# Optimization experiments

Hardware: AMD Instinct MI355X
Metric: run time of the kernel (lower is better)

## Reference

```python
import jax, jax.numpy as jnp
import numpy as np

C = 1024
H = 16
EPS = 1e-5

def layernorm(x, g, b):
    mu = jnp.mean(x, axis=-1, keepdims=True)
    var = jnp.var(x, axis=-1, keepdims=True)
    return (x - mu) * jax.lax.rsqrt(var + EPS) * g + b

def setup_inputs() -> dict:
    key = jax.random.key(0)
    ks = jax.random.split(key, 12)
    s = lambda fan: 1.0 / np.sqrt(fan)
    return {
        "x": jax.random.normal(ks[0], (2, 2048, C), jnp.float32),
        "W_qkv": jax.random.uniform(ks[1], (C, 3 * C), jnp.float32, -s(C), s(C)),
        "W_o": jax.random.uniform(ks[2], (C, C), jnp.float32, -s(C), s(C)),
        "b_o": jnp.zeros((C,), jnp.float32),
        "g1": jnp.ones((C,), jnp.float32),
        "beta1": jnp.zeros((C,), jnp.float32),
        "g2": jnp.ones((C,), jnp.float32),
        "beta2": jnp.zeros((C,), jnp.float32),
        "W_ff1": jax.random.uniform(ks[3], (C, 4 * C), jnp.float32, -s(C), s(C)),
        "b_ff1": jnp.zeros((4 * C,), jnp.float32),
        "W_ff2": jax.random.uniform(ks[4], (4 * C, C), jnp.float32, -s(4 * C), s(4 * C)),
        "b_ff2": jnp.zeros((C,), jnp.float32),
    }

def reference(x, W_qkv, W_o, b_o, g1, beta1, g2, beta2, W_ff1, b_ff1, W_ff2, b_ff2):
    B, T, _ = x.shape
    hd = C // H  # head dim
    # --- self-attention on norm1(x) ---
    h = layernorm(x, g1, beta1)
    qkv = h @ W_qkv                      # [B,T,3C]
    q, k, v = jnp.split(qkv, 3, axis=-1)
    reshp = lambda t: t.reshape(B, T, H, hd).transpose(0, 2, 1, 3)  # [B,H,T,hd]
    q, k, v = reshp(q), reshp(k), reshp(v)
    att = jnp.einsum("bhqd,bhkd->bhqk", q, k) * (hd ** -0.5)
    causal = jnp.tril(jnp.ones((T, T), bool))
    att = jnp.where(causal, att, -jnp.inf)
    att = jax.nn.softmax(att, axis=-1)
    out = jnp.einsum("bhqk,bhkd->bhqd", att, v)
    out = out.transpose(0, 2, 1, 3).reshape(B, T, C)
    x = x + out @ W_o + b_o
    # --- feed-forward on norm2(x) ---
    h = layernorm(x, g2, beta2)
    h = jax.nn.relu(h @ W_ff1 + b_ff1) @ W_ff2 + b_ff2
    return x + h
```

## Files before the change

### kernel.cpp

```cpp
#include <hip/hip_runtime.h>
#include <hip/hip_bf16.h>
#include <stdint.h>


typedef __attribute__((ext_vector_type(8))) short bf16x8;
typedef __attribute__((ext_vector_type(4))) float f32x4;

#define MFMA16(a, b, c) __builtin_amdgcn_mfma_f32_16x16x32_bf16((a), (b), (c), 0, 0, 0)

__device__ __forceinline__ void gload16(const void* g, void* l) {
    __builtin_amdgcn_global_load_lds(
        (const __attribute__((address_space(1))) char*)g,
        (__attribute__((address_space(3))) char*)l, 16, 0, 0);
}

__global__ __launch_bounds__(256) void tconv_k(const float* __restrict__ in,
                                               __hip_bfloat16* __restrict__ out,
                                               int K, int N) {
    __shared__ float tile[32][33];
    const int n0 = blockIdx.x * 32, k0 = blockIdx.y * 32;
    const int tx = threadIdx.x, ty = threadIdx.y;
    for (int i = ty; i < 32; i += 8)
        tile[i][tx] = in[(size_t)(k0 + i) * N + n0 + tx];
    __syncthreads();
    for (int i = ty; i < 32; i += 8)
        out[(size_t)(n0 + i) * K + k0 + tx] = __float2bfloat16(tile[tx][i]);
}

__global__ __launch_bounds__(256) void ln_k(const float* __restrict__ x,
                                            const float* __restrict__ g,
                                            const float* __restrict__ beta,
                                            __hip_bfloat16* __restrict__ out) {
    const int row = blockIdx.x;
    const int tid = threadIdx.x;
    float4 v = ((const float4*)(x + (size_t)row * 1024))[tid];
    float s  = v.x + v.y + v.z + v.w;
    float s2 = v.x * v.x + v.y * v.y + v.z * v.z + v.w * v.w;
    for (int off = 1; off < 64; off <<= 1) {
        s  += __shfl_xor(s,  off, 64);
        s2 += __shfl_xor(s2, off, 64);
    }
    __shared__ float ss[4], ss2[4];
    const int w = tid >> 6, lane = tid & 63;
    if (lane == 0) { ss[w] = s; ss2[w] = s2; }
    __syncthreads();
    s  = ss[0] + ss[1] + ss[2] + ss[3];
    s2 = ss2[0] + ss2[1] + ss2[2] + ss2[3];
    const float mu  = s * (1.0f / 1024.0f);
    const float var = s2 * (1.0f / 1024.0f) - mu * mu;
    const float rs  = rsqrtf(var + 1e-5f);
    float4 gv = ((const float4*)g)[tid];
    float4 bv = ((const float4*)beta)[tid];
    __hip_bfloat16* o = out + (size_t)row * 1024 + tid * 4;
    o[0] = __float2bfloat16((v.x - mu) * rs * gv.x + bv.x);
    o[1] = __float2bfloat16((v.y - mu) * rs * gv.y + bv.y);
    o[2] = __float2bfloat16((v.z - mu) * rs * gv.z + bv.z);
    o[3] = __float2bfloat16((v.w - mu) * rs * gv.w + bv.w);
}

template <int BIAS, int RELU, int RESID, int OUTBF>
__global__ __launch_bounds__(256, 3) void gemm_k(const __hip_bfloat16* __restrict__ A,
                                                 const __hip_bfloat16* __restrict__ Bt,
                                                 const float* __restrict__ bias,
                                                 const float* __restrict__ resid,
                                                 void* __restrict__ out,
                                                 int M, int N, int K) {
    __align__(16) __shared__ __hip_bfloat16 As[128 * 64];
    __align__(16) __shared__ __hip_bfloat16 Bs[128 * 64];

    const int tid  = threadIdx.x;
    const int lane = tid & 63, w = tid >> 6;
    const int wm = w >> 1, wn = w & 1;
    const int m0 = blockIdx.y * 128, n0 = blockIdx.x * 128;
    const int l16 = lane & 15, quad = lane >> 4;

    const int srw = lane >> 3;
    const int scn = ((lane & 7) - srw) & 7;

    const __hip_bfloat16* ga[4];
    const __hip_bfloat16* gb[4];
#pragma unroll
    for (int i = 0; i < 4; i++) {
        const int row = i * 32 + w * 8 + srw;
        ga[i] = A  + (size_t)(m0 + row) * K + scn * 8;
        gb[i] = Bt + (size_t)(n0 + row) * K + scn * 8;
    }

    int offA[2][4], offB[2][4];
#pragma unroll
    for (int s = 0; s < 2; s++)
#pragma unroll
        for (int t = 0; t < 4; t++) {
            const int rA = wm * 64 + t * 16 + l16;
            offA[s][t] = (rA * 8 + ((s * 4 + quad + (rA & 7)) & 7)) * 16;
            const int rB = wn * 64 + t * 16 + l16;
            offB[s][t] = (rB * 8 + ((s * 4 + quad + (rB & 7)) & 7)) * 16;
        }

    f32x4 acc[4][4] = {};

    for (int k0 = 0; k0 < K; k0 += 64) {
        __syncthreads();
#pragma unroll
        for (int i = 0; i < 4; i++) {
            gload16(ga[i], As + (i * 256 + w * 64) * 8);
            gload16(gb[i], Bs + (i * 256 + w * 64) * 8);
            ga[i] += 64; gb[i] += 64;
        }
        __syncthreads();

#pragma unroll
        for (int s = 0; s < 2; s++) {
            bf16x8 af[4], bfr[4];
#pragma unroll
            for (int t = 0; t < 4; t++) {
                af[t]  = *(const bf16x8*)((const char*)As + offA[s][t]);
                bfr[t] = *(const bf16x8*)((const char*)Bs + offB[s][t]);
            }
#pragma unroll
            for (int mt = 0; mt < 4; mt++)
#pragma unroll
                for (int nt = 0; nt < 4; nt++)
                    acc[mt][nt] = MFMA16(af[mt], bfr[nt], acc[mt][nt]);
        }
    }

#pragma unroll
    for (int mt = 0; mt < 4; mt++)
#pragma unroll
        for (int nt = 0; nt < 4; nt++) {
            const int row = m0 + wm * 64 + mt * 16 + quad * 4;
            const int col = n0 + wn * 64 + nt * 16 + l16;
            const float bv = BIAS ? bias[col] : 0.0f;
#pragma unroll
            for (int r = 0; r < 4; r++) {
                float v = acc[mt][nt][r] + bv;
                if (RELU) v = v > 0.0f ? v : 0.0f;
                const size_t idx = (size_t)(row + r) * N + col;
                if (RESID) v += resid[idx];
                if (OUTBF) ((__hip_bfloat16*)out)[idx] = __float2bfloat16(v);
                else       ((float*)out)[idx] = v;
            }
        }
}

template <int BIAS, int RELU, int RESID, int OUTBF>
__global__ __launch_bounds__(256, 3) void gemm64_k(const __hip_bfloat16* __restrict__ A,
                                                   const __hip_bfloat16* __restrict__ Bt,
                                                   const float* __restrict__ bias,
                                                   const float* __restrict__ resid,
                                                   void* __restrict__ out,
                                                   int M, int N, int K) {
    __align__(16) __shared__ __hip_bfloat16 As[128 * 64];
    __align__(16) __shared__ __hip_bfloat16 Bs[64 * 64];

    const int tid  = threadIdx.x;
    const int lane = tid & 63, w = tid >> 6;
    const int wm = w >> 1, wn = w & 1;
    const int m0 = blockIdx.y * 128, n0 = blockIdx.x * 64;
    const int l16 = lane & 15, quad = lane >> 4;

    const int srw = lane >> 3;
    const int scn = ((lane & 7) - srw) & 7;

    const __hip_bfloat16* ga[4];
    const __hip_bfloat16* gb[2];
#pragma unroll
    for (int i = 0; i < 4; i++)
        ga[i] = A + (size_t)(m0 + i * 32 + w * 8 + srw) * K + scn * 8;
#pragma unroll
    for (int i = 0; i < 2; i++)
        gb[i] = Bt + (size_t)(n0 + i * 32 + w * 8 + srw) * K + scn * 8;

    int offA[2][4], offB[2][2];
#pragma unroll
    for (int s = 0; s < 2; s++) {
#pragma unroll
        for (int t = 0; t < 4; t++) {
            const int rA = wm * 64 + t * 16 + l16;
            offA[s][t] = (rA * 8 + ((s * 4 + quad + (rA & 7)) & 7)) * 16;
        }
#pragma unroll
        for (int t = 0; t < 2; t++) {
            const int rB = wn * 32 + t * 16 + l16;
            offB[s][t] = (rB * 8 + ((s * 4 + quad + (rB & 7)) & 7)) * 16;
        }
    }

    f32x4 acc[4][2] = {};

    for (int k0 = 0; k0 < K; k0 += 64) {
        __syncthreads();
#pragma unroll
        for (int i = 0; i < 4; i++) {
            gload16(ga[i], As + (i * 256 + w * 64) * 8);
            ga[i] += 64;
        }
#pragma unroll
        for (int i = 0; i < 2; i++) {
            gload16(gb[i], Bs + (i * 256 + w * 64) * 8);
            gb[i] += 64;
        }
        __syncthreads();

#pragma unroll
        for (int s = 0; s < 2; s++) {
            bf16x8 af[4], bfr[2];
#pragma unroll
            for (int t = 0; t < 4; t++)
                af[t] = *(const bf16x8*)((const char*)As + offA[s][t]);
#pragma unroll
            for (int t = 0; t < 2; t++)
                bfr[t] = *(const bf16x8*)((const char*)Bs + offB[s][t]);
#pragma unroll
            for (int mt = 0; mt < 4; mt++)
#pragma unroll
                for (int nt = 0; nt < 2; nt++)
                    acc[mt][nt] = MFMA16(af[mt], bfr[nt], acc[mt][nt]);
        }
    }

#pragma unroll
    for (int mt = 0; mt < 4; mt++)
#pragma unroll
        for (int nt = 0; nt < 2; nt++) {
            const int row = m0 + wm * 64 + mt * 16 + quad * 4;
            const int col = n0 + wn * 32 + nt * 16 + l16;
            const float bv = BIAS ? bias[col] : 0.0f;
#pragma unroll
            for (int r = 0; r < 4; r++) {
                float v = acc[mt][nt][r] + bv;
                if (RELU) v = v > 0.0f ? v : 0.0f;
                const size_t idx = (size_t)(row + r) * N + col;
                if (RESID) v += resid[idx];
                if (OUTBF) ((__hip_bfloat16*)out)[idx] = __float2bfloat16(v);
                else       ((float*)out)[idx] = v;
            }
        }
}

__global__ __launch_bounds__(256) void vtrans_k(const __hip_bfloat16* __restrict__ qkv,
                                                __hip_bfloat16* __restrict__ vt) {
    const int T = 2048, C3 = 3072;
    const int bh = blockIdx.y, b = bh >> 4, h = bh & 15;
    const int t0 = blockIdx.x * 64;
    const int tx = threadIdx.x, ty = threadIdx.y;
    __shared__ __hip_bfloat16 tile[64][65];
#pragma unroll
    for (int j = 0; j < 16; j++) {
        const int tl = ty * 16 + j;
        tile[tl][tx] = qkv[(size_t)(b * T + t0 + tl) * C3 + 2048 + h * 64 + tx];
    }
    __syncthreads();
#pragma unroll
    for (int j = 0; j < 16; j++) {
        const int d = ty * 16 + j;
        vt[((size_t)bh * 64 + d) * 2048 + t0 + tx] = tile[tx][d];
    }
}

__global__ __launch_bounds__(256, 3) void attn_k(const __hip_bfloat16* __restrict__ qkv,
                                                 const __hip_bfloat16* __restrict__ vt,
                                                 __hip_bfloat16* __restrict__ outp) {
    const int T = 2048, C3 = 3072;
    const int bh = blockIdx.x, b = bh >> 4, h = bh & 15;
    const int qt = 31 - blockIdx.y;
    const int q0 = qt * 64;
    const int tid = threadIdx.x, lane = tid & 63, w = tid >> 6;
    const int l16 = lane & 15, quad = lane >> 4;

    __align__(16) __shared__ __hip_bfloat16 Ks[2][64 * 64];
    __align__(16) __shared__ __hip_bfloat16 Vs[2][64 * 64];
    __align__(16) __shared__ __hip_bfloat16 Pw[4][16 * 72];

    const float sc = 0.125f * 1.44269504f;
    bf16x8 qf0, qf1;
    {
        const __hip_bfloat16* qp =
            qkv + (size_t)(b * T + q0 + w * 16 + l16) * C3 + h * 64;
        bf16x8 a = *(const bf16x8*)(qp + quad * 8);
        bf16x8 c = *(const bf16x8*)(qp + 32 + quad * 8);
#pragma unroll
        for (int i = 0; i < 8; i++) {
            union { unsigned int u; float f; } ua, uc;
            ua.u = ((unsigned int)(unsigned short)a[i]) << 16;
            uc.u = ((unsigned int)(unsigned short)c[i]) << 16;
            qf0[i] = (short)(__bfloat16_as_ushort(__float2bfloat16(ua.f * sc)));
            qf1[i] = (short)(__bfloat16_as_ushort(__float2bfloat16(uc.f * sc)));
        }
    }

    const int srw = lane >> 3;
    const int scn = ((lane & 7) - srw) & 7;
    const __hip_bfloat16* kp[2];
    const __hip_bfloat16* vp[2];
#pragma unroll
    for (int i = 0; i < 2; i++) {
        const int row = i * 32 + w * 8 + srw;
        kp[i] = qkv + (size_t)(b * T + row) * C3 + 1024 + h * 64 + scn * 8;
        vp[i] = vt + ((size_t)bh * 64 + row) * 2048 + scn * 8;
    }

    int offK[2][4], offV[2][4];
#pragma unroll
    for (int s = 0; s < 2; s++)
#pragma unroll
        for (int t = 0; t < 4; t++) {
            const int rr = t * 16 + l16;
            const int o = (rr * 8 + ((s * 4 + quad + (rr & 7)) & 7)) * 16;
            offK[s][t] = o;
            offV[s][t] = o;
        }

    f32x4 oacc[4] = {};
    float lpart[4] = {0.0f, 0.0f, 0.0f, 0.0f};

#pragma unroll
    for (int i = 0; i < 2; i++) {
        gload16(kp[i], Ks[0] + (i * 256 + w * 64) * 8);
        gload16(vp[i], Vs[0] + (i * 256 + w * 64) * 8);
    }

    for (int kt = 0; kt <= qt; kt++) {
        const int buf = kt & 1;
        __syncthreads();
        if (kt < qt) {
#pragma unroll
            for (int i = 0; i < 2; i++) {
                gload16(kp[i] + (size_t)(kt + 1) * 64 * C3,
                        Ks[buf ^ 1] + (i * 256 + w * 64) * 8);
                gload16(vp[i] + (kt + 1) * 64,
                        Vs[buf ^ 1] + (i * 256 + w * 64) * 8);
            }
        }

        f32x4 s4[4];
#pragma unroll
        for (int nt = 0; nt < 4; nt++) {
            bf16x8 kf0 = *(const bf16x8*)((const char*)Ks[buf] + offK[0][nt]);
            bf16x8 kf1 = *(const bf16x8*)((const char*)Ks[buf] + offK[1][nt]);
            f32x4 z = {};
            z = MFMA16(qf0, kf0, z);
            z = MFMA16(qf1, kf1, z);
            s4[nt] = z;
        }

        const bool diag = (kt == qt);
        const int myrow = w * 16 + quad * 4;
#pragma unroll
        for (int nt = 0; nt < 4; nt++) {
            const int col = nt * 16 + l16;
#pragma unroll
            for (int r = 0; r < 4; r++) {
                float p = exp2f(s4[nt][r]);
                if (diag && col > myrow + r) p = 0.0f;
                lpart[r] += p;
                Pw[w][(quad * 4 + r) * 72 + col] = __float2bfloat16(p);
            }
        }

        asm volatile("s_waitcnt lgkmcnt(0)" ::: "memory");

        bf16x8 pf0 = *(const bf16x8*)(&Pw[w][l16 * 72 + quad * 8]);
        bf16x8 pf1 = *(const bf16x8*)(&Pw[w][l16 * 72 + 32 + quad * 8]);
#pragma unroll
        for (int dt = 0; dt < 4; dt++) {
            bf16x8 vf0 = *(const bf16x8*)((const char*)Vs[buf] + offV[0][dt]);
            bf16x8 vf1 = *(const bf16x8*)((const char*)Vs[buf] + offV[1][dt]);
            oacc[dt] = MFMA16(pf0, vf0, oacc[dt]);
            oacc[dt] = MFMA16(pf1, vf1, oacc[dt]);
        }
    }

#pragma unroll
    for (int off = 1; off < 16; off <<= 1)
#pragma unroll
        for (int r = 0; r < 4; r++)
            lpart[r] += __shfl_xor(lpart[r], off, 64);

    float rl[4];
#pragma unroll
    for (int r = 0; r < 4; r++) rl[r] = 1.0f / lpart[r];
#pragma unroll
    for (int dt = 0; dt < 4; dt++)
#pragma unroll
        for (int r = 0; r < 4; r++) {
            const int row = q0 + w * 16 + quad * 4 + r;
            outp[(size_t)(b * T + row) * 1024 + h * 64 + dt * 16 + l16] =
                __float2bfloat16(oacc[dt][r] * rl[r]);
        }
}

extern "C" void kernel_launch(void* const* d_in, const int* in_sizes, int n_in,
                              void* d_out, int out_size, void* d_ws, size_t ws_size,
                              hipStream_t stream) {
    const float* x     = (const float*)d_in[0];
    const float* Wqkv  = (const float*)d_in[1];
    const float* Wo    = (const float*)d_in[2];
    const float* b_o   = (const float*)d_in[3];
    const float* g1    = (const float*)d_in[4];
    const float* beta1 = (const float*)d_in[5];
    const float* g2    = (const float*)d_in[6];
    const float* beta2 = (const float*)d_in[7];
    const float* Wff1  = (const float*)d_in[8];
    const float* bff1  = (const float*)d_in[9];
    const float* Wff2  = (const float*)d_in[10];
    const float* bff2  = (const float*)d_in[11];

    char* ws = (char*)d_ws;
    size_t off = 0;
    auto alloc = [&](size_t bytes) {
        void* p = ws + off;
        off += (bytes + 255) & ~(size_t)255;
        return p;
    };
    __hip_bfloat16* Wqkv_t = (__hip_bfloat16*)alloc(3072ULL * 1024 * 2);
    __hip_bfloat16* Wo_t   = (__hip_bfloat16*)alloc(1024ULL * 1024 * 2);
    __hip_bfloat16* Wff1_t = (__hip_bfloat16*)alloc(4096ULL * 1024 * 2);
    __hip_bfloat16* Wff2_t = (__hip_bfloat16*)alloc(1024ULL * 4096 * 2);
    __hip_bfloat16* h_bf   = (__hip_bfloat16*)alloc(4096ULL * 1024 * 2);
    __hip_bfloat16* qkv_bf = (__hip_bfloat16*)alloc(4096ULL * 3072 * 2);
    __hip_bfloat16* att_bf = (__hip_bfloat16*)alloc(4096ULL * 1024 * 2);
    float*          x2     = (float*)alloc(4096ULL * 1024 * 4);
    __hip_bfloat16* ff1_bf = qkv_bf;
    __hip_bfloat16* vt     = (__hip_bfloat16*)x2;

    const dim3 tb(32, 8);
    tconv_k<<<dim3(3072 / 32, 1024 / 32), tb, 0, stream>>>(Wqkv, Wqkv_t, 1024, 3072);
    tconv_k<<<dim3(1024 / 32, 1024 / 32), tb, 0, stream>>>(Wo,   Wo_t,   1024, 1024);
    tconv_k<<<dim3(4096 / 32, 1024 / 32), tb, 0, stream>>>(Wff1, Wff1_t, 1024, 4096);
    tconv_k<<<dim3(1024 / 32, 4096 / 32), tb, 0, stream>>>(Wff2, Wff2_t, 4096, 1024);

    ln_k<<<4096, 256, 0, stream>>>(x, g1, beta1, h_bf);
    gemm_k<0, 0, 0, 1><<<dim3(3072 / 128, 4096 / 128), 256, 0, stream>>>(
        h_bf, Wqkv_t, nullptr, nullptr, qkv_bf, 4096, 3072, 1024);
    vtrans_k<<<dim3(32, 32), dim3(64, 4), 0, stream>>>(qkv_bf, vt);
    attn_k<<<dim3(32, 32), 256, 0, stream>>>(qkv_bf, vt, att_bf);
    gemm64_k<1, 0, 1, 0><<<dim3(1024 / 64, 4096 / 128), 256, 0, stream>>>(
        att_bf, Wo_t, b_o, x, x2, 4096, 1024, 1024);
    ln_k<<<4096, 256, 0, stream>>>(x2, g2, beta2, h_bf);
    gemm_k<1, 1, 0, 1><<<dim3(4096 / 128, 4096 / 128), 256, 0, stream>>>(
        h_bf, Wff1_t, bff1, nullptr, ff1_bf, 4096, 4096, 1024);
    gemm64_k<1, 0, 1, 0><<<dim3(1024 / 64, 4096 / 128), 256, 0, stream>>>(
        ff1_bf, Wff2_t, bff2, x2, (float*)d_out, 4096, 1024, 4096);
}
```

Measured before the change: 346.1 us.

## Double-buffer LDS tiles in GEMM kernels to overlap global loads with MFMA

```diff
diff --git a/kernel.cpp b/kernel.cpp
--- a/kernel.cpp
+++ b/kernel.cpp
@@ -59,14 +59,14 @@
 }
 
 template <int BIAS, int RELU, int RESID, int OUTBF>
-__global__ __launch_bounds__(256, 3) void gemm_k(const __hip_bfloat16* __restrict__ A,
+__global__ __launch_bounds__(256, 2) void gemm_k(const __hip_bfloat16* __restrict__ A,
                                                  const __hip_bfloat16* __restrict__ Bt,
                                                  const float* __restrict__ bias,
                                                  const float* __restrict__ resid,
                                                  void* __restrict__ out,
                                                  int M, int N, int K) {
-    __align__(16) __shared__ __hip_bfloat16 As[128 * 64];
-    __align__(16) __shared__ __hip_bfloat16 Bs[128 * 64];
+    __align__(16) __shared__ __hip_bfloat16 As[2][128 * 64];
+    __align__(16) __shared__ __hip_bfloat16 Bs[2][128 * 64];
 
     const int tid  = threadIdx.x;
     const int lane = tid & 63, w = tid >> 6;
@@ -99,23 +99,33 @@
 
     f32x4 acc[4][4] = {};
 
-    for (int k0 = 0; k0 < K; k0 += 64) {
+#pragma unroll
+    for (int i = 0; i < 4; i++) {
+        gload16(ga[i], As[0] + (i * 256 + w * 64) * 8);
+        gload16(gb[i], Bs[0] + (i * 256 + w * 64) * 8);
+        ga[i] += 64; gb[i] += 64;
+    }
+
+    const int niter = K >> 6;
+    for (int it = 0; it < niter; it++) {
+        const int buf = it & 1;
         __syncthreads();
-#pragma unroll
-        for (int i = 0; i < 4; i++) {
-            gload16(ga[i], As + (i * 256 + w * 64) * 8);
-            gload16(gb[i], Bs + (i * 256 + w * 64) * 8);
-            ga[i] += 64; gb[i] += 64;
-        }
-        __syncthreads();
+        if (it + 1 < niter) {
+#pragma unroll
+            for (int i = 0; i < 4; i++) {
+                gload16(ga[i], As[buf ^ 1] + (i * 256 + w * 64) * 8);
+                gload16(gb[i], Bs[buf ^ 1] + (i * 256 + w * 64) * 8);
+                ga[i] += 64; gb[i] += 64;
+            }
+        }
 
 #pragma unroll
         for (int s = 0; s < 2; s++) {
             bf16x8 af[4], bfr[4];
 #pragma unroll
             for (int t = 0; t < 4; t++) {
-                af[t]  = *(const bf16x8*)((const char*)As + offA[s][t]);
-                bfr[t] = *(const bf16x8*)((const char*)Bs + offB[s][t]);
+                af[t]  = *(const bf16x8*)((const char*)As[buf] + offA[s][t]);
+                bfr[t] = *(const bf16x8*)((const char*)Bs[buf] + offB[s][t]);
             }
 #pragma unroll
             for (int mt = 0; mt < 4; mt++)
@@ -151,8 +161,8 @@
                                                    const float* __restrict__ resid,
                                                    void* __restrict__ out,
                                                    int M, int N, int K) {
-    __align__(16) __shared__ __hip_bfloat16 As[128 * 64];
-    __align__(16) __shared__ __hip_bfloat16 Bs[64 * 64];
+    __align__(16) __shared__ __hip_bfloat16 As[2][128 * 64];
+    __align__(16) __shared__ __hip_bfloat16 Bs[2][64 * 64];
 
     const int tid  = threadIdx.x;
     const int lane = tid & 63, w = tid >> 6;
@@ -189,29 +199,43 @@
 
     f32x4 acc[4][2] = {};
 
-    for (int k0 = 0; k0 < K; k0 += 64) {
+#pragma unroll
+    for (int i = 0; i < 4; i++) {
+        gload16(ga[i], As[0] + (i * 256 + w * 64) * 8);
+        ga[i] += 64;
+    }
+#pragma unroll
+    for (int i = 0; i < 2; i++) {
+        gload16(gb[i], Bs[0] + (i * 256 + w * 64) * 8);
+        gb[i] += 64;
+    }
+
+    const int niter = K >> 6;
+    for (int it = 0; it < niter; it++) {
+        const int buf = it & 1;
         __syncthreads();
-#pragma unroll
-        for (int i = 0; i < 4; i++) {
-            gload16(ga[i], As + (i * 256 + w * 64) * 8);
-            ga[i] += 64;
-        }
-#pragma unroll
-        for (int i = 0; i < 2; i++) {
-            gload16(gb[i], Bs + (i * 256 + w * 64) * 8);
-            gb[i] += 64;
-        }
-        __syncthreads();
+        if (it + 1 < niter) {
+#pragma unroll
+            for (int i = 0; i < 4; i++) {
+                gload16(ga[i], As[buf ^ 1] + (i * 256 + w * 64) * 8);
+                ga[i] += 64;
+            }
+#pragma unroll
+            for (int i = 0; i < 2; i++) {
+                gload16(gb[i], Bs[buf ^ 1] + (i * 256 + w * 64) * 8);
+                gb[i] += 64;
+            }
+        }
 
 #pragma unroll
         for (int s = 0; s < 2; s++) {
             bf16x8 af[4], bfr[2];
 #pragma unroll
             for (int t = 0; t < 4; t++)
-                af[t] = *(const bf16x8*)((const char*)As + offA[s][t]);
+                af[t] = *(const bf16x8*)((const char*)As[buf] + offA[s][t]);
 #pragma unroll
             for (int t = 0; t < 2; t++)
-                bfr[t] = *(const bf16x8*)((const char*)Bs + offB[s][t]);
+                bfr[t] = *(const bf16x8*)((const char*)Bs[buf] + offB[s][t]);
 #pragma unroll
             for (int mt = 0; mt < 4; mt++)
 #pragma unroll
@@ -301,15 +325,13 @@
         vp[i] = vt + ((size_t)bh * 64 + row) * 2048 + scn * 8;
     }
 
-    int offK[2][4], offV[2][4];
+    int offK[2][4];
 #pragma unroll
     for (int s = 0; s < 2; s++)
 #pragma unroll
         for (int t = 0; t < 4; t++) {
             const int rr = t * 16 + l16;
-            const int o = (rr * 8 + ((s * 4 + quad + (rr & 7)) & 7)) * 16;
-            offK[s][t] = o;
-            offV[s][t] = o;
+            offK[s][t] = (rr * 8 + ((s * 4 + quad + (rr & 7)) & 7)) * 16;
         }
 
     f32x4 oacc[4] = {};
@@ -365,8 +387,8 @@
         bf16x8 pf1 = *(const bf16x8*)(&Pw[w][l16 * 72 + 32 + quad * 8]);
 #pragma unroll
         for (int dt = 0; dt < 4; dt++) {
-            bf16x8 vf0 = *(const bf16x8*)((const char*)Vs[buf] + offV[0][dt]);
-            bf16x8 vf1 = *(const bf16x8*)((const char*)Vs[buf] + offV[1][dt]);
+            bf16x8 vf0 = *(const bf16x8*)((const char*)Vs[buf] + offK[0][dt]);
+            bf16x8 vf1 = *(const bf16x8*)((const char*)Vs[buf] + offK[1][dt]);
             oacc[dt] = MFMA16(pf0, vf0, oacc[dt]);
             oacc[dt] = MFMA16(pf1, vf1, oacc[dt]);
         }
```

Result: no change. 340.6 us (-1.6%).
